# Optimization experiments

Hardware: AMD Instinct MI355X
Metric: run time of the kernel (lower is better)

## Reference

```python
import jax, jax.numpy as jnp
import numpy as np

N_NODES = 50000
N_EDGES = 800000
IN_DIM = 256
HID = 64
NEG_SLOPE = 0.2


def setup_inputs() -> dict:
    key = jax.random.key(0)
    ks = jax.random.split(key, 16)
    s = lambda d: 1.0 / np.sqrt(d)
    x = jax.random.normal(ks[0], (N_NODES, IN_DIM), dtype=jnp.float32)
    src = jax.random.randint(ks[1], (N_EDGES,), 0, N_NODES, dtype=jnp.int32)
    dst = jax.random.randint(ks[2], (N_EDGES,), 0, N_NODES, dtype=jnp.int32)
    # layer 0: in 256 -> 4 heads x 64, no residual, ELU
    W0 = jax.random.normal(ks[3], (IN_DIM, 4 * HID), dtype=jnp.float32) * s(IN_DIM)
    al0 = jax.random.normal(ks[4], (4, HID), dtype=jnp.float32) * s(HID)
    ar0 = jax.random.normal(ks[5], (4, HID), dtype=jnp.float32) * s(HID)
    b0 = jnp.zeros((4 * HID,), dtype=jnp.float32)
    # layer 1: in 256 -> 4 heads x 64, identity residual (256 == 4*64), ELU
    W1 = jax.random.normal(ks[6], (4 * HID, 4 * HID), dtype=jnp.float32) * s(4 * HID)
    al1 = jax.random.normal(ks[7], (4, HID), dtype=jnp.float32) * s(HID)
    ar1 = jax.random.normal(ks[8], (4, HID), dtype=jnp.float32) * s(HID)
    b1 = jnp.zeros((4 * HID,), dtype=jnp.float32)
    # layer 2 (output): in 256 -> 1 head x 64, linear residual, no activation
    W2 = jax.random.normal(ks[9], (4 * HID, HID), dtype=jnp.float32) * s(4 * HID)
    al2 = jax.random.normal(ks[10], (1, HID), dtype=jnp.float32) * s(HID)
    ar2 = jax.random.normal(ks[11], (1, HID), dtype=jnp.float32) * s(HID)
    b2 = jnp.zeros((HID,), dtype=jnp.float32)
    res_w2 = jax.random.normal(ks[12], (4 * HID, HID), dtype=jnp.float32) * s(4 * HID)
    return {"x": x, "src": src, "dst": dst,
            "W0": W0, "al0": al0, "ar0": ar0, "b0": b0,
            "W1": W1, "al1": al1, "ar1": ar1, "b1": b1,
            "W2": W2, "al2": al2, "ar2": ar2, "b2": b2,
            "res_w2": res_w2}


def gat_layer(h, src, dst, W, al, ar, bias, residual, res_w, activation):
    H, D = al.shape
    feat = (h @ W).reshape(-1, H, D)               # [N,H,D]
    el = jnp.sum(feat * al[None], axis=-1)         # [N,H]
    er = jnp.sum(feat * ar[None], axis=-1)         # [N,H]
    e = jax.nn.leaky_relu(el[src] + er[dst], NEG_SLOPE)  # [E,H]
    # segment softmax over incoming edges of each destination node
    emax = jax.ops.segment_max(e, dst, num_segments=N_NODES)  # [N,H]
    ee = jnp.exp(e - emax[dst])
    denom = jax.ops.segment_sum(ee, dst, num_segments=N_NODES)
    alpha = ee / denom[dst]                        # [E,H]
    msg = feat[src] * alpha[..., None]             # [E,H,D]
    out = jax.ops.segment_sum(msg, dst, num_segments=N_NODES)  # [N,H,D]
    if residual:
        if res_w is not None:
            out = out + (h @ res_w).reshape(-1, 1, D)
        else:
            out = out + h.reshape(-1, H, D)
    out = out + bias.reshape(H, D)
    if activation:
        out = jax.nn.elu(out)
    return out.reshape(-1, H * D)                  # flatten(1)


def reference(x, src, dst, W0, al0, ar0, b0, W1, al1, ar1, b1,
              W2, al2, ar2, b2, res_w2):
    h = gat_layer(x, src, dst, W0, al0, ar0, b0, False, None, True)
    h = gat_layer(h, src, dst, W1, al1, ar1, b1, True, None, True)
    h = gat_layer(h, src, dst, W2, al2, ar2, b2, True, res_w2, False)
    return h  # [N, 64]
```

## Files before the change

### kernel.cpp

```cpp
#include <hip/hip_runtime.h>
#include <math.h>

#define NNODES 50000
#define NEDGES 800000
#define NSB 49
#define NPACK 640
#define NCVT 3125
#define EBH 3125
#define NBM 391
#define SCB 1563

__device__ __forceinline__ float leaky(float x) { return x > 0.f ? x : 0.2f * x; }

__device__ __forceinline__ ushort f2bf(float f) {
    unsigned u = __float_as_uint(f);
    return (ushort)((u + 0x7fffu + ((u >> 16) & 1u)) >> 16);
}
__device__ __forceinline__ float bf2f(ushort u) {
    return __uint_as_float((unsigned)u << 16);
}

typedef const __attribute__((address_space(1))) void* gptr_t;
typedef __attribute__((address_space(3))) void* lptr_t;

__global__ __launch_bounds__(256) void front_kernel(
    const int* __restrict__ dst, int* __restrict__ counts,
    const float* __restrict__ W0, const float* __restrict__ W1, const float* __restrict__ W2,
    const float* __restrict__ Wr, ushort* __restrict__ Bt0, ushort* __restrict__ Bt1,
    ushort* __restrict__ Bt2, const float* __restrict__ x, ushort* __restrict__ xb) {
    using ushort8v = __attribute__((ext_vector_type(8))) unsigned short;
    int t = threadIdx.x;
    if (blockIdx.x < EBH) {
        int e = blockIdx.x * 256 + t;
        if (e < NEDGES) atomicAdd(&counts[dst[e]], 1);
    } else if (blockIdx.x < EBH + NPACK) {
        int idx = (blockIdx.x - EBH) * 256 + t;
        if (idx < 65536) {
            int n = idx >> 8, k = idx & 255;
            Bt0[idx] = f2bf(W0[k * 256 + n]);
        } else if (idx < 131072) {
            int j = idx - 65536;
            int n = j >> 8, k = j & 255;
            Bt1[j] = f2bf(W1[k * 256 + n]);
        } else {
            int j = idx - 131072;
            int n = j >> 8, k = j & 255;
            Bt2[j] = f2bf(n < 64 ? W2[k * 64 + n] : Wr[k * 64 + (n - 64)]);
        }
    } else {
        size_t j = (size_t)(blockIdx.x - EBH - NPACK) * 4096 + t * 16;
        float4 a0 = *reinterpret_cast<const float4*>(x + j);
        float4 a1 = *reinterpret_cast<const float4*>(x + j + 4);
        float4 a2 = *reinterpret_cast<const float4*>(x + j + 8);
        float4 a3 = *reinterpret_cast<const float4*>(x + j + 12);
        union { ushort8v v; ushort u[8]; } p0, p1;
        p0.u[0] = f2bf(a0.x); p0.u[1] = f2bf(a0.y); p0.u[2] = f2bf(a0.z); p0.u[3] = f2bf(a0.w);
        p0.u[4] = f2bf(a1.x); p0.u[5] = f2bf(a1.y); p0.u[6] = f2bf(a1.z); p0.u[7] = f2bf(a1.w);
        p1.u[0] = f2bf(a2.x); p1.u[1] = f2bf(a2.y); p1.u[2] = f2bf(a2.z); p1.u[3] = f2bf(a2.w);
        p1.u[4] = f2bf(a3.x); p1.u[5] = f2bf(a3.y); p1.u[6] = f2bf(a3.z); p1.u[7] = f2bf(a3.w);
        *reinterpret_cast<ushort8v*>(xb + j) = p0.v;
        *reinterpret_cast<ushort8v*>(xb + j + 8) = p1.v;
    }
}

__global__ __launch_bounds__(256) void scan_partial(const int* __restrict__ counts,
                                                    int* __restrict__ bsum, int Nn) {
    int b = blockIdx.x, t = threadIdx.x;
    int base = b * 1024;
    int v = 0;
#pragma unroll
    for (int i = 0; i < 4; ++i) {
        int idx = base + t + 256 * i;
        if (idx < Nn) v += counts[idx];
    }
    for (int o = 32; o; o >>= 1) v += __shfl_xor(v, o);
    __shared__ int ws[4];
    if ((t & 63) == 0) ws[t >> 6] = v;
    __syncthreads();
    if (t == 0) bsum[b] = ws[0] + ws[1] + ws[2] + ws[3];
}

__global__ __launch_bounds__(256) void scan_final(const int* __restrict__ counts,
                                                  const int* __restrict__ bsum,
                                                  int* __restrict__ row_start, int Nn, int nB) {
    __shared__ int off_s;
    __shared__ int tsum[256];
    int b = blockIdx.x, t = threadIdx.x;
    if (t == 0) {
        int o = 0;
        for (int i = 0; i < b; ++i) o += bsum[i];
        off_s = o;
    }
    int base = b * 1024 + t * 4;
    int c0 = 0, c1 = 0, c2 = 0, c3 = 0;
    if (base + 3 < Nn) {
        int4 c = *reinterpret_cast<const int4*>(counts + base);
        c0 = c.x; c1 = c.y; c2 = c.z; c3 = c.w;
    } else {
        if (base + 0 < Nn) c0 = counts[base + 0];
        if (base + 1 < Nn) c1 = counts[base + 1];
        if (base + 2 < Nn) c2 = counts[base + 2];
        if (base + 3 < Nn) c3 = counts[base + 3];
    }
    int s0 = c0, s1 = s0 + c1, s2 = s1 + c2, s3 = s2 + c3;
    tsum[t] = s3;
    __syncthreads();
    for (int o = 1; o < 256; o <<= 1) {
        int u = (t >= o) ? tsum[t - o] : 0;
        __syncthreads();
        tsum[t] += u;
        __syncthreads();
    }
    int o = off_s + tsum[t] - s3;
    if (base + 3 < Nn) {
        *reinterpret_cast<int4*>(row_start + base) = make_int4(o, o + s0, o + s1, o + s2);
    } else {
        if (base + 0 < Nn) row_start[base + 0] = o;
        if (base + 1 < Nn) row_start[base + 1] = o + s0;
        if (base + 2 < Nn) row_start[base + 2] = o + s1;
        if (base + 3 < Nn) row_start[base + 3] = o + s2;
    }
    if (b == nB - 1 && t == 255) row_start[Nn] = off_s + tsum[255];
}

template <bool SCAT>
__global__ __launch_bounds__(512) void gemm_wide(const ushort* __restrict__ Ab,
                                                 const ushort* __restrict__ Bt,
                                                 const float* __restrict__ al,
                                                 const float* __restrict__ ar,
                                                 ushort* __restrict__ featb,
                                                 float* __restrict__ el, float* __restrict__ er,
                                                 int Nrows,
                                                 const int* __restrict__ srcv,
                                                 const int* __restrict__ dstv,
                                                 const int* __restrict__ row_start,
                                                 int* __restrict__ cursor,
                                                 int* __restrict__ csr_src) {
    using bf16x8 = __attribute__((ext_vector_type(8))) short;
    using f32x4 = __attribute__((ext_vector_type(4))) float;
    __shared__ ushort As[8192];
    __shared__ ushort Bs[16384];
    if constexpr (SCAT) {
        if (blockIdx.x >= NBM) {
            int e = (blockIdx.x - NBM) * 512 + threadIdx.x;
            if (e < NEDGES) {
                int d = dstv[e];
                int pos = row_start[d] + atomicAdd(&cursor[d], 1);
                csr_src[pos] = srcv[e];
            }
            return;
        }
    }
    const int tid = threadIdx.x;
    const int lane = tid & 63;
    const int wave = tid >> 6;
    const int wr = wave >> 2, wc = wave & 3;
    const int q = lane >> 4, li = lane & 15;
    const int r0 = blockIdx.x * 128;

    f32x4 acc[4][4];
#pragma unroll
    for (int i = 0; i < 4; ++i)
#pragma unroll
        for (int j = 0; j < 4; ++j) acc[i][j] = (f32x4){0.f, 0.f, 0.f, 0.f};

    for (int kk = 0; kk < 256; kk += 64) {
        __syncthreads();
#pragma unroll
        for (int j = 0; j < 2; ++j) {
            int c = wave * 128 + j * 64 + lane;
            int mr = c & 15, kg = (c >> 4) & 7, mf = c >> 7;
            const ushort* gp = Ab + (size_t)(r0 + mf * 16 + mr) * 256 + kk + kg * 8;
            void* lp = (char*)As + (size_t)(wave * 2 + j) * 1024;
            __builtin_amdgcn_global_load_lds((gptr_t)gp, (lptr_t)lp, 16, 0, 0);
        }
#pragma unroll
        for (int j = 0; j < 4; ++j) {
            int c = wave * 256 + j * 64 + lane;
            int nr = c & 15, kg = (c >> 4) & 7, nf = c >> 7;
            const ushort* gp = Bt + (size_t)(nf * 16 + nr) * 256 + kk + kg * 8;
            void* lp = (char*)Bs + (size_t)(wave * 4 + j) * 1024;
            __builtin_amdgcn_global_load_lds((gptr_t)gp, (lptr_t)lp, 16, 0, 0);
        }
        __syncthreads();
#pragma unroll
        for (int t = 0; t < 2; ++t) {
            const int kc = t * 4 + q;
            bf16x8 af[4], bfv[4];
#pragma unroll
            for (int f = 0; f < 4; ++f) {
                af[f] = *reinterpret_cast<const bf16x8*>(
                    &As[(((wr * 4 + f) * 8 + kc) * 16 + li) * 8]);
                bfv[f] = *reinterpret_cast<const bf16x8*>(
                    &Bs[(((wc * 4 + f) * 8 + kc) * 16 + li) * 8]);
            }
#pragma unroll
            for (int f = 0; f < 4; ++f)
#pragma unroll
                for (int f2 = 0; f2 < 4; ++f2)
                    acc[f][f2] =
                        __builtin_amdgcn_mfma_f32_16x16x32_bf16(af[f], bfv[f2], acc[f][f2], 0, 0, 0);
        }
    }

    float alv[4], arv[4];
#pragma unroll
    for (int f2 = 0; f2 < 4; ++f2) {
        alv[f2] = al[wc * 64 + f2 * 16 + li];
        arv[f2] = ar[wc * 64 + f2 * 16 + li];
    }
#pragma unroll
    for (int f = 0; f < 4; ++f) {
#pragma unroll
        for (int r = 0; r < 4; ++r) {
            int row = r0 + wr * 64 + f * 16 + q * 4 + r;
            bool ok = row < Nrows;
            float elp = 0.f, erp = 0.f;
#pragma unroll
            for (int f2 = 0; f2 < 4; ++f2) {
                float v = acc[f][f2][r];
                elp = fmaf(v, alv[f2], elp);
                erp = fmaf(v, arv[f2], erp);
                if (ok) featb[(size_t)row * 256 + (f2 * 16 + li) * 4 + wc] = f2bf(v);
            }
#pragma unroll
            for (int o = 1; o < 16; o <<= 1) {
                elp += __shfl_xor(elp, o);
                erp += __shfl_xor(erp, o);
            }
            if (ok && li == 0) {
                el[row * 4 + wc] = elp;
                er[row * 4 + wc] = erp;
            }
        }
    }
}

__global__ __launch_bounds__(256) void gemm_l2(const ushort* __restrict__ Ab,
                                               const ushort* __restrict__ Bt,
                                               const float* __restrict__ al,
                                               const float* __restrict__ ar,
                                               ushort* __restrict__ featb,
                                               float* __restrict__ el, float* __restrict__ er,
                                               float* __restrict__ resid, int Nrows) {
    using bf16x8 = __attribute__((ext_vector_type(8))) short;
    using f32x4 = __attribute__((ext_vector_type(4))) float;
    __shared__ ushort As[8192];
    __shared__ ushort Bs[8192];
    const int tid = threadIdx.x;
    const int lane = tid & 63;
    const int wave = tid >> 6;
    const int wr = wave >> 1, wc = wave & 1;
    const int q = lane >> 4, li = lane & 15;
    const int r0 = blockIdx.x * 128;

    f32x4 acc[4][4];
#pragma unroll
    for (int i = 0; i < 4; ++i)
#pragma unroll
        for (int j = 0; j < 4; ++j) acc[i][j] = (f32x4){0.f, 0.f, 0.f, 0.f};

    for (int kk = 0; kk < 256; kk += 64) {
        __syncthreads();
#pragma unroll
        for (int j = 0; j < 4; ++j) {
            int c = (wave * 4 + j) * 64 + lane;
            int mr = c & 15, kg = (c >> 4) & 7, mf = c >> 7;
            const ushort* gp = Ab + (size_t)(r0 + mf * 16 + mr) * 256 + kk + kg * 8;
            void* lp = (char*)As + (size_t)(wave * 4 + j) * 1024;
            __builtin_amdgcn_global_load_lds((gptr_t)gp, (lptr_t)lp, 16, 0, 0);
        }
#pragma unroll
        for (int j = 0; j < 4; ++j) {
            int c = (wave * 4 + j) * 64 + lane;
            int nr = c & 15, kg = (c >> 4) & 7, nf = c >> 7;
            const ushort* gp = Bt + (size_t)(nf * 16 + nr) * 256 + kk + kg * 8;
            void* lp = (char*)Bs + (size_t)(wave * 4 + j) * 1024;
            __builtin_amdgcn_global_load_lds((gptr_t)gp, (lptr_t)lp, 16, 0, 0);
        }
        __syncthreads();
#pragma unroll
        for (int t = 0; t < 2; ++t) {
            const int kc = t * 4 + q;
            bf16x8 af[4], bfv[4];
#pragma unroll
            for (int f = 0; f < 4; ++f) {
                af[f] = *reinterpret_cast<const bf16x8*>(
                    &As[(((wr * 4 + f) * 8 + kc) * 16 + li) * 8]);
                bfv[f] = *reinterpret_cast<const bf16x8*>(
                    &Bs[(((wc * 4 + f) * 8 + kc) * 16 + li) * 8]);
            }
#pragma unroll
            for (int f = 0; f < 4; ++f)
#pragma unroll
                for (int f2 = 0; f2 < 4; ++f2)
                    acc[f][f2] =
                        __builtin_amdgcn_mfma_f32_16x16x32_bf16(af[f], bfv[f2], acc[f][f2], 0, 0, 0);
        }
    }

    if (wc == 0) {
        float alv[4], arv[4];
#pragma unroll
        for (int f2 = 0; f2 < 4; ++f2) {
            alv[f2] = al[f2 * 16 + li];
            arv[f2] = ar[f2 * 16 + li];
        }
#pragma unroll
        for (int f = 0; f < 4; ++f) {
#pragma unroll
            for (int r = 0; r < 4; ++r) {
                int row = r0 + wr * 64 + f * 16 + q * 4 + r;
                bool ok = row < Nrows;
                float elp = 0.f, erp = 0.f;
#pragma unroll
                for (int f2 = 0; f2 < 4; ++f2) {
                    float v = acc[f][f2][r];
                    elp = fmaf(v, alv[f2], elp);
                    erp = fmaf(v, arv[f2], erp);
                    if (ok) featb[(size_t)row * 64 + f2 * 16 + li] = f2bf(v);
                }
#pragma unroll
                for (int o = 1; o < 16; o <<= 1) {
                    elp += __shfl_xor(elp, o);
                    erp += __shfl_xor(erp, o);
                }
                if (ok && li == 0) {
                    el[row] = elp;
                    er[row] = erp;
                }
            }
        }
    } else {
#pragma unroll
        for (int f = 0; f < 4; ++f) {
#pragma unroll
            for (int r = 0; r < 4; ++r) {
                int row = r0 + wr * 64 + f * 16 + q * 4 + r;
                if (row < Nrows) {
#pragma unroll
                    for (int f2 = 0; f2 < 4; ++f2)
                        resid[(size_t)row * 64 + f2 * 16 + li] = acc[f][f2][r];
                }
            }
        }
    }
}

template <int RES, bool ACT>
__global__ __launch_bounds__(256) void agg4_kernel(
    const ushort* __restrict__ featb, const float* __restrict__ el,
    const float* __restrict__ er, const int* __restrict__ row_start,
    const int* __restrict__ csr_src, const ushort* __restrict__ resbuf,
    const float* __restrict__ bias, ushort* __restrict__ out, int Nn) {
    using ushort8v = __attribute__((ext_vector_type(8))) unsigned short;
    __shared__ float wbuf[4][256];
    __shared__ int obuf[4][64];
    const int wv = threadIdx.x >> 6, lane = threadIdx.x & 63;
    const int g = lane >> 5, li = lane & 31;
    int node = blockIdx.x * 4 + wv;
    if (node >= Nn) return;

    int begin = row_start[node], end = row_start[node + 1];
    float4 ern = *(reinterpret_cast<const float4*>(er) + node);

    float denom[4] = {0.f, 0.f, 0.f, 0.f};
    float acc[2][4] = {{0.f, 0.f, 0.f, 0.f}, {0.f, 0.f, 0.f, 0.f}};

    for (int c = begin; c < end; c += 64) {
        int nE = min(64, end - c);
        float4 w = make_float4(0.f, 0.f, 0.f, 0.f);
        int s = 0;
        if (lane < nE) {
            s = csr_src[c + lane];
            float4 e4 = *(reinterpret_cast<const float4*>(el) + s);
            w.x = __expf(leaky(e4.x + ern.x));
            w.y = __expf(leaky(e4.y + ern.y));
            w.z = __expf(leaky(e4.z + ern.z));
            w.w = __expf(leaky(e4.w + ern.w));
        }
        denom[0] += w.x; denom[1] += w.y; denom[2] += w.z; denom[3] += w.w;
        obuf[wv][lane] = s * 256;
        *reinterpret_cast<float4*>(&wbuf[wv][lane * 4]) = w;
        __asm__ volatile("s_waitcnt lgkmcnt(0)" ::: "memory");

#pragma unroll 4
        for (int e2 = 0; e2 < nE; e2 += 2) {
            int e = e2 + g;
            float4 we = make_float4(0.f, 0.f, 0.f, 0.f);
            int off = 0;
            if (e < nE) {
                off = obuf[wv][e];
                we = *reinterpret_cast<const float4*>(&wbuf[wv][e * 4]);
            }
            ushort8v v = *reinterpret_cast<const ushort8v*>(featb + off + li * 8);
            acc[0][0] = fmaf(we.x, bf2f(v[0]), acc[0][0]);
            acc[0][1] = fmaf(we.y, bf2f(v[1]), acc[0][1]);
            acc[0][2] = fmaf(we.z, bf2f(v[2]), acc[0][2]);
            acc[0][3] = fmaf(we.w, bf2f(v[3]), acc[0][3]);
            acc[1][0] = fmaf(we.x, bf2f(v[4]), acc[1][0]);
            acc[1][1] = fmaf(we.y, bf2f(v[5]), acc[1][1]);
            acc[1][2] = fmaf(we.z, bf2f(v[6]), acc[1][2]);
            acc[1][3] = fmaf(we.w, bf2f(v[7]), acc[1][3]);
        }
        __asm__ volatile("" ::: "memory");
    }

#pragma unroll
    for (int j = 0; j < 2; ++j)
#pragma unroll
        for (int h = 0; h < 4; ++h) acc[j][h] += __shfl_xor(acc[j][h], 32);
#pragma unroll
    for (int h = 0; h < 4; ++h)
        for (int o = 32; o; o >>= 1) denom[h] += __shfl_xor(denom[h], o);

    bool has = end > begin;
#pragma unroll
    for (int hh = 0; hh < 2; ++hh) {
        int h = g * 2 + hh;
        float d0 = denom[h];
        float o0 = has ? acc[0][h] / d0 : 0.f;
        float o1 = has ? acc[1][h] / d0 : 0.f;
        int dbase = h * 64 + li * 2;
        if constexpr (RES == 1) {
            unsigned rv = *reinterpret_cast<const unsigned*>(resbuf + (size_t)node * 256 + dbase);
            o0 += bf2f((ushort)(rv & 0xffffu));
            o1 += bf2f((ushort)(rv >> 16));
        }
        float2 bv = *reinterpret_cast<const float2*>(bias + dbase);
        o0 += bv.x; o1 += bv.y;
        if constexpr (ACT) {
            o0 = o0 > 0.f ? o0 : __expf(o0) - 1.f;
            o1 = o1 > 0.f ? o1 : __expf(o1) - 1.f;
        }
        unsigned pk = (unsigned)f2bf(o0) | ((unsigned)f2bf(o1) << 16);
        *reinterpret_cast<unsigned*>(out + (size_t)node * 256 + dbase) = pk;
    }
}

__global__ __launch_bounds__(256) void agg1_kernel(
    const ushort* __restrict__ featb, const float* __restrict__ el,
    const float* __restrict__ er, const int* __restrict__ row_start,
    const int* __restrict__ csr_src, const float* __restrict__ resbuf,
    const float* __restrict__ bias, float* __restrict__ out, int Nn) {
    __shared__ float wbuf[4][64];
    __shared__ int obuf[4][64];
    const int wv = threadIdx.x >> 6, lane = threadIdx.x & 63;
    const int g = lane >> 4, li = lane & 15;
    int node = blockIdx.x * 4 + wv;
    if (node >= Nn) return;

    int begin = row_start[node], end = row_start[node + 1];
    float ern = er[node];
    float denom = 0.f;
    float acc[4] = {0.f, 0.f, 0.f, 0.f};

    for (int c = begin; c < end; c += 64) {
        int nE = min(64, end - c);
        float w = 0.f;
        int s = 0;
        if (lane < nE) {
            s = csr_src[c + lane];
            w = __expf(leaky(el[s] + ern));
        }
        denom += w;
        obuf[wv][lane] = s * 64;
        wbuf[wv][lane] = w;
        __asm__ volatile("s_waitcnt lgkmcnt(0)" ::: "memory");

#pragma unroll 2
        for (int e4i = 0; e4i < nE; e4i += 4) {
            int e = e4i + g;
            float we = 0.f;
            int off = 0;
            if (e < nE) {
                off = obuf[wv][e];
                we = wbuf[wv][e];
            }
            ushort4 v = *reinterpret_cast<const ushort4*>(featb + off + li * 4);
            acc[0] = fmaf(we, bf2f(v.x), acc[0]);
            acc[1] = fmaf(we, bf2f(v.y), acc[1]);
            acc[2] = fmaf(we, bf2f(v.z), acc[2]);
            acc[3] = fmaf(we, bf2f(v.w), acc[3]);
        }
        __asm__ volatile("" ::: "memory");
    }

#pragma unroll
    for (int j = 0; j < 4; ++j) {
        acc[j] += __shfl_xor(acc[j], 16);
        acc[j] += __shfl_xor(acc[j], 32);
    }
    for (int o = 32; o; o >>= 1) denom += __shfl_xor(denom, o);

    if (g == 0) {
        bool has = end > begin;
        float4 rv = *reinterpret_cast<const float4*>(resbuf + (size_t)node * 64 + li * 4);
        float4 bv = *reinterpret_cast<const float4*>(bias + li * 4);
        float4 o4;
        o4.x = (has ? acc[0] / denom : 0.f) + rv.x + bv.x;
        o4.y = (has ? acc[1] / denom : 0.f) + rv.y + bv.y;
        o4.z = (has ? acc[2] / denom : 0.f) + rv.z + bv.z;
        o4.w = (has ? acc[3] / denom : 0.f) + rv.w + bv.w;
        *reinterpret_cast<float4*>(out + (size_t)node * 64 + li * 4) = o4;
    }
}

extern "C" void kernel_launch(void* const* d_in, const int* in_sizes, int n_in, void* d_out,
                              int out_size, void* d_ws, size_t ws_size, hipStream_t stream) {
    const float* x   = (const float*)d_in[0];
    const int* src   = (const int*)d_in[1];
    const int* dst   = (const int*)d_in[2];
    const float* W0  = (const float*)d_in[3];
    const float* al0 = (const float*)d_in[4];
    const float* ar0 = (const float*)d_in[5];
    const float* b0  = (const float*)d_in[6];
    const float* W1  = (const float*)d_in[7];
    const float* al1 = (const float*)d_in[8];
    const float* ar1 = (const float*)d_in[9];
    const float* b1  = (const float*)d_in[10];
    const float* W2  = (const float*)d_in[11];
    const float* al2 = (const float*)d_in[12];
    const float* ar2 = (const float*)d_in[13];
    const float* b2  = (const float*)d_in[14];
    const float* Wr2 = (const float*)d_in[15];
    float* out = (float*)d_out;

    char* w = (char*)d_ws;
    size_t off = 0;
    auto alloc = [&](size_t bytes) -> char* {
        char* p = w + off;
        off += (bytes + 255) & ~(size_t)255;
        return p;
    };
    ushort* xb      = (ushort*)alloc((size_t)NNODES * 256 * 2);
    ushort* hbuf    = (ushort*)alloc((size_t)NNODES * 256 * 2);
    ushort* featb   = (ushort*)alloc((size_t)NNODES * 256 * 2);
    float* resid    = (float*)alloc((size_t)NNODES * 64 * 4);
    float* el       = (float*)alloc((size_t)NNODES * 4 * 4);
    float* er       = (float*)alloc((size_t)NNODES * 4 * 4);
    ushort* Bt0     = (ushort*)alloc(65536 * 2);
    ushort* Bt1     = (ushort*)alloc(65536 * 2);
    ushort* Bt2     = (ushort*)alloc(32768 * 2);
    int* counts     = (int*)alloc((size_t)NNODES * 4 * 2);
    int* cursor     = counts + NNODES;
    int* row_start  = (int*)alloc((size_t)(NNODES + 1) * 4);
    int* bsum       = (int*)alloc(64 * 4);
    int* csr_src    = (int*)alloc((size_t)NEDGES * 4);

    hipMemsetAsync(counts, 0, (size_t)NNODES * 4 * 2, stream);

    const int NB4 = (NNODES + 3) / 4;

    front_kernel<<<EBH + NPACK + NCVT, 256, 0, stream>>>(dst, counts, W0, W1, W2, Wr2,
                                                         Bt0, Bt1, Bt2, x, xb);
    scan_partial<<<NSB, 256, 0, stream>>>(counts, bsum, NNODES);
    scan_final<<<NSB, 256, 0, stream>>>(counts, bsum, row_start, NNODES, NSB);

    gemm_wide<true><<<NBM + SCB, 512, 0, stream>>>(xb, Bt0, al0, ar0, featb, el, er, NNODES,
                                                   src, dst, row_start, cursor, csr_src);
    agg4_kernel<0, true><<<NB4, 256, 0, stream>>>(featb, el, er, row_start, csr_src,
                                                  nullptr, b0, hbuf, NNODES);
    gemm_wide<false><<<NBM, 512, 0, stream>>>(hbuf, Bt1, al1, ar1, featb, el, er, NNODES,
                                              nullptr, nullptr, nullptr, nullptr, nullptr);
    agg4_kernel<1, true><<<NB4, 256, 0, stream>>>(featb, el, er, row_start, csr_src,
                                                  hbuf, b1, hbuf, NNODES);
    gemm_l2<<<NBM, 256, 0, stream>>>(hbuf, Bt2, al2, ar2, featb, el, er, resid, NNODES);
    agg1_kernel<<<NB4, 256, 0, stream>>>(featb, el, er, row_start, csr_src,
                                         resid, b2, out, NNODES);
}
```

Baseline: 419.4 us.

## Store features in column slabs and split aggregation by column group per XCD

Node features and the bf16 input are stored as 8 column slabs of 32 channels each, instead of row-major 256-wide rows. The GEMM loads and stores are re-indexed to match. The aggregation kernels now launch one block per (16-node group, column slab), with the slab chosen by blockIdx&7. Each block therefore gathers from a 3.2MB slab, which should fit in cache and, with round-robin block dispatch, mostly map to one XCD's L2. CSR source indices shrink to 16-bit to cut index traffic. In exchange, the edge-softmax weights (exp) are recomputed once per slab, and the 16-bit indices only work because there are fewer than 65536 nodes.

Result: slower. 629.1 us (+50.0%).

```diff
diff --git a/kernel.cpp b/kernel.cpp
--- a/kernel.cpp
+++ b/kernel.cpp
@@ -9,6 +9,8 @@
 #define EBH 3125
 #define NBM 391
 #define SCB 1563
+#define AGG4B 25000
+#define AGG1B 6250
 
 __device__ __forceinline__ float leaky(float x) { return x > 0.f ? x : 0.2f * x; }
 
@@ -22,6 +24,7 @@
 
 typedef const __attribute__((address_space(1))) void* gptr_t;
 typedef __attribute__((address_space(3))) void* lptr_t;
+
 
 __global__ __launch_bounds__(256) void front_kernel(
     const int* __restrict__ dst, int* __restrict__ counts,
@@ -49,6 +52,8 @@
         }
     } else {
         size_t j = (size_t)(blockIdx.x - EBH - NPACK) * 4096 + t * 16;
+        int node = (int)(j >> 8);
+        int c0 = (int)(j & 255);
         float4 a0 = *reinterpret_cast<const float4*>(x + j);
         float4 a1 = *reinterpret_cast<const float4*>(x + j + 4);
         float4 a2 = *reinterpret_cast<const float4*>(x + j + 8);
@@ -58,8 +63,11 @@
         p0.u[4] = f2bf(a1.x); p0.u[5] = f2bf(a1.y); p0.u[6] = f2bf(a1.z); p0.u[7] = f2bf(a1.w);
         p1.u[0] = f2bf(a2.x); p1.u[1] = f2bf(a2.y); p1.u[2] = f2bf(a2.z); p1.u[3] = f2bf(a2.w);
         p1.u[4] = f2bf(a3.x); p1.u[5] = f2bf(a3.y); p1.u[6] = f2bf(a3.z); p1.u[7] = f2bf(a3.w);
-        *reinterpret_cast<ushort8v*>(xb + j) = p0.v;
-        *reinterpret_cast<ushort8v*>(xb + j + 8) = p1.v;
+        int c1 = c0 + 8;
+        size_t o0 = ((size_t)((c0 >> 3) & 7) * NNODES + node) * 32 + ((c0 >> 6) << 3);
+        size_t o1 = ((size_t)((c1 >> 3) & 7) * NNODES + node) * 32 + ((c1 >> 6) << 3);
+        *reinterpret_cast<ushort8v*>(xb + o0) = p0.v;
+        *reinterpret_cast<ushort8v*>(xb + o1) = p1.v;
     }
 }
 
@@ -135,7 +143,7 @@
                                                  const int* __restrict__ dstv,
                                                  const int* __restrict__ row_start,
                                                  int* __restrict__ cursor,
-                                                 int* __restrict__ csr_src) {
+                                                 ushort* __restrict__ csr_src) {
     using bf16x8 = __attribute__((ext_vector_type(8))) short;
     using f32x4 = __attribute__((ext_vector_type(4))) float;
     __shared__ ushort As[8192];
@@ -146,7 +154,7 @@
             if (e < NEDGES) {
                 int d = dstv[e];
                 int pos = row_start[d] + atomicAdd(&cursor[d], 1);
-                csr_src[pos] = srcv[e];
+                csr_src[pos] = (ushort)srcv[e];
             }
             return;
         }
@@ -170,7 +178,9 @@
         for (int j = 0; j < 2; ++j) {
             int c = wave * 128 + j * 64 + lane;
             int mr = c & 15, kg = (c >> 4) & 7, mf = c >> 7;
-            const ushort* gp = Ab + (size_t)(r0 + mf * 16 + mr) * 256 + kk + kg * 8;
+            int k0 = kk + kg * 8;
+            int row = r0 + mf * 16 + mr;
+            const ushort* gp = Ab + ((size_t)((k0 >> 3) & 7) * NNODES + row) * 32 + ((k0 >> 6) << 3);
             void* lp = (char*)As + (size_t)(wave * 2 + j) * 1024;
             __builtin_amdgcn_global_load_lds((gptr_t)gp, (lptr_t)lp, 16, 0, 0);
         }
@@ -221,7 +231,8 @@
                 float v = acc[f][f2][r];
                 elp = fmaf(v, alv[f2], elp);
                 erp = fmaf(v, arv[f2], erp);
-                if (ok) featb[(size_t)row * 256 + (f2 * 16 + li) * 4 + wc] = f2bf(v);
+                int cc = (f2 * 16 + li) * 4 + wc;
+                if (ok) featb[((size_t)(cc >> 5) * NNODES + row) * 32 + (cc & 31)] = f2bf(v);
             }
 #pragma unroll
             for (int o = 1; o < 16; o <<= 1) {
@@ -266,7 +277,9 @@
         for (int j = 0; j < 4; ++j) {
             int c = (wave * 4 + j) * 64 + lane;
             int mr = c & 15, kg = (c >> 4) & 7, mf = c >> 7;
-            const ushort* gp = Ab + (size_t)(r0 + mf * 16 + mr) * 256 + kk + kg * 8;
+            int k0 = kk + kg * 8;
+            int row = r0 + mf * 16 + mr;
+            const ushort* gp = Ab + ((size_t)((k0 >> 3) & 7) * NNODES + row) * 32 + ((k0 >> 6) << 3);
             void* lp = (char*)As + (size_t)(wave * 4 + j) * 1024;
             __builtin_amdgcn_global_load_lds((gptr_t)gp, (lptr_t)lp, 16, 0, 0);
         }
@@ -318,7 +331,8 @@
                     float v = acc[f][f2][r];
                     elp = fmaf(v, alv[f2], elp);
                     erp = fmaf(v, arv[f2], erp);
-                    if (ok) featb[(size_t)row * 64 + f2 * 16 + li] = f2bf(v);
+                    int cc = f2 * 16 + li;
+                    if (ok) featb[((size_t)(cc >> 5) * NNODES + row) * 32 + (cc & 31)] = f2bf(v);
                 }
 #pragma unroll
                 for (int o = 1; o < 16; o <<= 1) {
@@ -348,161 +362,150 @@
 }
 
 template <int RES, bool ACT>
-__global__ __launch_bounds__(256) void agg4_kernel(
+__global__ __launch_bounds__(256) void agg4s_kernel(
     const ushort* __restrict__ featb, const float* __restrict__ el,
     const float* __restrict__ er, const int* __restrict__ row_start,
-    const int* __restrict__ csr_src, const ushort* __restrict__ resbuf,
-    const float* __restrict__ bias, ushort* __restrict__ out, int Nn) {
-    using ushort8v = __attribute__((ext_vector_type(8))) unsigned short;
-    __shared__ float wbuf[4][256];
+    const ushort* __restrict__ csr_src, const ushort* __restrict__ resbuf,
+    const float* __restrict__ bias, ushort* __restrict__ out) {
+    __shared__ float4 wbuf[4][64];
     __shared__ int obuf[4][64];
     const int wv = threadIdx.x >> 6, lane = threadIdx.x & 63;
-    const int g = lane >> 5, li = lane & 31;
-    int node = blockIdx.x * 4 + wv;
-    if (node >= Nn) return;
-
-    int begin = row_start[node], end = row_start[node + 1];
-    float4 ern = *(reinterpret_cast<const float4*>(er) + node);
-
-    float denom[4] = {0.f, 0.f, 0.f, 0.f};
-    float acc[2][4] = {{0.f, 0.f, 0.f, 0.f}, {0.f, 0.f, 0.f, 0.f}};
-
-    for (int c = begin; c < end; c += 64) {
-        int nE = min(64, end - c);
-        float4 w = make_float4(0.f, 0.f, 0.f, 0.f);
-        int s = 0;
-        if (lane < nE) {
-            s = csr_src[c + lane];
-            float4 e4 = *(reinterpret_cast<const float4*>(el) + s);
-            w.x = __expf(leaky(e4.x + ern.x));
-            w.y = __expf(leaky(e4.y + ern.y));
-            w.z = __expf(leaky(e4.z + ern.z));
-            w.w = __expf(leaky(e4.w + ern.w));
-        }
-        denom[0] += w.x; denom[1] += w.y; denom[2] += w.z; denom[3] += w.w;
-        obuf[wv][lane] = s * 256;
-        *reinterpret_cast<float4*>(&wbuf[wv][lane * 4]) = w;
-        __asm__ volatile("s_waitcnt lgkmcnt(0)" ::: "memory");
-
+    const int g = lane >> 3, li = lane & 7;
+    const int cg = blockIdx.x & 7;
+    const int blk = blockIdx.x >> 3;
+    const ushort* fslab = featb + (size_t)cg * NNODES * 32 + li * 4;
+    float bv = 0.f;
+    if (lane < 32) bv = bias[(lane >> 3) * 64 + cg * 8 + (lane & 7)];
+
+    for (int rep = 0; rep < 4; ++rep) {
+        const int node = blk * 16 + wv * 4 + rep;
+        const int begin = row_start[node], end = row_start[node + 1];
+        const float4 ern = *(reinterpret_cast<const float4*>(er) + node);
+        float dn[4] = {0.f, 0.f, 0.f, 0.f};
+        float acc[4] = {0.f, 0.f, 0.f, 0.f};
+        for (int c = begin; c < end; c += 64) {
+            int nE = min(64, end - c);
+            float4 w = make_float4(0.f, 0.f, 0.f, 0.f);
+            int s = 0;
+            if (lane < nE) {
+                s = csr_src[c + lane];
+                float4 e4 = *(reinterpret_cast<const float4*>(el) + s);
+                w.x = __expf(leaky(e4.x + ern.x));
+                w.y = __expf(leaky(e4.y + ern.y));
+                w.z = __expf(leaky(e4.z + ern.z));
+                w.w = __expf(leaky(e4.w + ern.w));
+            }
+            obuf[wv][lane] = s * 32;
+            wbuf[wv][lane] = w;
+            __asm__ volatile("s_waitcnt lgkmcnt(0)" ::: "memory");
 #pragma unroll 4
-        for (int e2 = 0; e2 < nE; e2 += 2) {
-            int e = e2 + g;
-            float4 we = make_float4(0.f, 0.f, 0.f, 0.f);
-            int off = 0;
-            if (e < nE) {
-                off = obuf[wv][e];
-                we = *reinterpret_cast<const float4*>(&wbuf[wv][e * 4]);
-            }
-            ushort8v v = *reinterpret_cast<const ushort8v*>(featb + off + li * 8);
-            acc[0][0] = fmaf(we.x, bf2f(v[0]), acc[0][0]);
-            acc[0][1] = fmaf(we.y, bf2f(v[1]), acc[0][1]);
-            acc[0][2] = fmaf(we.z, bf2f(v[2]), acc[0][2]);
-            acc[0][3] = fmaf(we.w, bf2f(v[3]), acc[0][3]);
-            acc[1][0] = fmaf(we.x, bf2f(v[4]), acc[1][0]);
-            acc[1][1] = fmaf(we.y, bf2f(v[5]), acc[1][1]);
-            acc[1][2] = fmaf(we.z, bf2f(v[6]), acc[1][2]);
-            acc[1][3] = fmaf(we.w, bf2f(v[7]), acc[1][3]);
-        }
-        __asm__ volatile("" ::: "memory");
-    }
-
-#pragma unroll
-    for (int j = 0; j < 2; ++j)
-#pragma unroll
-        for (int h = 0; h < 4; ++h) acc[j][h] += __shfl_xor(acc[j][h], 32);
-#pragma unroll
-    for (int h = 0; h < 4; ++h)
-        for (int o = 32; o; o >>= 1) denom[h] += __shfl_xor(denom[h], o);
-
-    bool has = end > begin;
-#pragma unroll
-    for (int hh = 0; hh < 2; ++hh) {
-        int h = g * 2 + hh;
-        float d0 = denom[h];
-        float o0 = has ? acc[0][h] / d0 : 0.f;
-        float o1 = has ? acc[1][h] / d0 : 0.f;
-        int dbase = h * 64 + li * 2;
-        if constexpr (RES == 1) {
-            unsigned rv = *reinterpret_cast<const unsigned*>(resbuf + (size_t)node * 256 + dbase);
-            o0 += bf2f((ushort)(rv & 0xffffu));
-            o1 += bf2f((ushort)(rv >> 16));
-        }
-        float2 bv = *reinterpret_cast<const float2*>(bias + dbase);
-        o0 += bv.x; o1 += bv.y;
-        if constexpr (ACT) {
-            o0 = o0 > 0.f ? o0 : __expf(o0) - 1.f;
-            o1 = o1 > 0.f ? o1 : __expf(o1) - 1.f;
-        }
-        unsigned pk = (unsigned)f2bf(o0) | ((unsigned)f2bf(o1) << 16);
-        *reinterpret_cast<unsigned*>(out + (size_t)node * 256 + dbase) = pk;
-    }
-}
-
-__global__ __launch_bounds__(256) void agg1_kernel(
+            for (int e8 = 0; e8 < nE; e8 += 8) {
+                int e = e8 + g;
+                float4 we = make_float4(0.f, 0.f, 0.f, 0.f);
+                int off = 0;
+                if (e < nE) {
+                    off = obuf[wv][e];
+                    we = wbuf[wv][e];
+                }
+                ushort4 v = *reinterpret_cast<const ushort4*>(fslab + off);
+                dn[0] += we.x; dn[1] += we.y; dn[2] += we.z; dn[3] += we.w;
+                acc[0] = fmaf(we.x, bf2f(v.x), acc[0]);
+                acc[1] = fmaf(we.y, bf2f(v.y), acc[1]);
+                acc[2] = fmaf(we.z, bf2f(v.z), acc[2]);
+                acc[3] = fmaf(we.w, bf2f(v.w), acc[3]);
+            }
+            __asm__ volatile("" ::: "memory");
+        }
+#pragma unroll
+        for (int h = 0; h < 4; ++h) {
+            acc[h] += __shfl_xor(acc[h], 8);
+            acc[h] += __shfl_xor(acc[h], 16);
+            acc[h] += __shfl_xor(acc[h], 32);
+            dn[h] += __shfl_xor(dn[h], 8);
+            dn[h] += __shfl_xor(dn[h], 16);
+            dn[h] += __shfl_xor(dn[h], 32);
+        }
+        if (lane < 32) {
+            const int h = lane >> 3;
+            float o = (end > begin) ? acc[h] * __builtin_amdgcn_rcpf(dn[h]) : 0.f;
+            size_t oidx = ((size_t)cg * NNODES + node) * 32 + lane;
+            if constexpr (RES == 1) o += bf2f(resbuf[oidx]);
+            o += bv;
+            if constexpr (ACT) o = o > 0.f ? o : __expf(o) - 1.f;
+            out[oidx] = f2bf(o);
+        }
+    }
+}
+
+__global__ __launch_bounds__(256) void agg1s_kernel(
     const ushort* __restrict__ featb, const float* __restrict__ el,
     const float* __restrict__ er, const int* __restrict__ row_start,
-    const int* __restrict__ csr_src, const float* __restrict__ resbuf,
-    const float* __restrict__ bias, float* __restrict__ out, int Nn) {
+    const ushort* __restrict__ csr_src, const float* __restrict__ resbuf,
+    const float* __restrict__ bias, float* __restrict__ out) {
     __shared__ float wbuf[4][64];
     __shared__ int obuf[4][64];
     const int wv = threadIdx.x >> 6, lane = threadIdx.x & 63;
-    const int g = lane >> 4, li = lane & 15;
-    int node = blockIdx.x * 4 + wv;
-    if (node >= Nn) return;
-
-    int begin = row_start[node], end = row_start[node + 1];
-    float ern = er[node];
-    float denom = 0.f;
-    float acc[4] = {0.f, 0.f, 0.f, 0.f};
-
-    for (int c = begin; c < end; c += 64) {
-        int nE = min(64, end - c);
-        float w = 0.f;
-        int s = 0;
-        if (lane < nE) {
-            s = csr_src[c + lane];
-            w = __expf(leaky(el[s] + ern));
-        }
-        denom += w;
-        obuf[wv][lane] = s * 64;
-        wbuf[wv][lane] = w;
-        __asm__ volatile("s_waitcnt lgkmcnt(0)" ::: "memory");
-
-#pragma unroll 2
-        for (int e4i = 0; e4i < nE; e4i += 4) {
-            int e = e4i + g;
-            float we = 0.f;
-            int off = 0;
-            if (e < nE) {
-                off = obuf[wv][e];
-                we = wbuf[wv][e];
-            }
-            ushort4 v = *reinterpret_cast<const ushort4*>(featb + off + li * 4);
-            acc[0] = fmaf(we, bf2f(v.x), acc[0]);
-            acc[1] = fmaf(we, bf2f(v.y), acc[1]);
-            acc[2] = fmaf(we, bf2f(v.z), acc[2]);
-            acc[3] = fmaf(we, bf2f(v.w), acc[3]);
-        }
-        __asm__ volatile("" ::: "memory");
-    }
-
-#pragma unroll
-    for (int j = 0; j < 4; ++j) {
-        acc[j] += __shfl_xor(acc[j], 16);
-        acc[j] += __shfl_xor(acc[j], 32);
-    }
-    for (int o = 32; o; o >>= 1) denom += __shfl_xor(denom, o);
-
-    if (g == 0) {
-        bool has = end > begin;
-        float4 rv = *reinterpret_cast<const float4*>(resbuf + (size_t)node * 64 + li * 4);
-        float4 bv = *reinterpret_cast<const float4*>(bias + li * 4);
-        float4 o4;
-        o4.x = (has ? acc[0] / denom : 0.f) + rv.x + bv.x;
-        o4.y = (has ? acc[1] / denom : 0.f) + rv.y + bv.y;
-        o4.z = (has ? acc[2] / denom : 0.f) + rv.z + bv.z;
-        o4.w = (has ? acc[3] / denom : 0.f) + rv.w + bv.w;
-        *reinterpret_cast<float4*>(out + (size_t)node * 64 + li * 4) = o4;
+    const int g = lane >> 3, li = lane & 7;
+    const int cg = blockIdx.x & 1;
+    const int blk = blockIdx.x >> 1;
+    const ushort* fslab = featb + (size_t)cg * NNODES * 32 + li * 4;
+    float4 bv = make_float4(0.f, 0.f, 0.f, 0.f);
+    if (lane < 8) bv = *reinterpret_cast<const float4*>(bias + cg * 32 + lane * 4);
+
+    for (int rep = 0; rep < 4; ++rep) {
+        const int node = blk * 16 + wv * 4 + rep;
+        const int begin = row_start[node], end = row_start[node + 1];
+        const float ern = er[node];
+        float dn = 0.f;
+        float acc[4] = {0.f, 0.f, 0.f, 0.f};
+        for (int c = begin; c < end; c += 64) {
+            int nE = min(64, end - c);
+            float w = 0.f;
+            int s = 0;
+            if (lane < nE) {
+                s = csr_src[c + lane];
+                w = __expf(leaky(el[s] + ern));
+            }
+            obuf[wv][lane] = s * 32;
+            wbuf[wv][lane] = w;
+            __asm__ volatile("s_waitcnt lgkmcnt(0)" ::: "memory");
+#pragma unroll 4
+            for (int e8 = 0; e8 < nE; e8 += 8) {
+                int e = e8 + g;
+                float we = 0.f;
+                int off = 0;
+                if (e < nE) {
+                    off = obuf[wv][e];
+                    we = wbuf[wv][e];
+                }
+                ushort4 v = *reinterpret_cast<const ushort4*>(fslab + off);
+                dn += we;
+                acc[0] = fmaf(we, bf2f(v.x), acc[0]);
+                acc[1] = fmaf(we, bf2f(v.y), acc[1]);
+                acc[2] = fmaf(we, bf2f(v.z), acc[2]);
+                acc[3] = fmaf(we, bf2f(v.w), acc[3]);
+            }
+            __asm__ volatile("" ::: "memory");
+        }
+#pragma unroll
+        for (int j = 0; j < 4; ++j) {
+            acc[j] += __shfl_xor(acc[j], 8);
+            acc[j] += __shfl_xor(acc[j], 16);
+            acc[j] += __shfl_xor(acc[j], 32);
+        }
+        dn += __shfl_xor(dn, 8);
+        dn += __shfl_xor(dn, 16);
+        dn += __shfl_xor(dn, 32);
+        if (lane < 8) {
+            float inv = (end > begin) ? __builtin_amdgcn_rcpf(dn) : 0.f;
+            float4 rv = *reinterpret_cast<const float4*>(resbuf + (size_t)node * 64 + cg * 32 + lane * 4);
+            float4 o4;
+            o4.x = acc[0] * inv + rv.x + bv.x;
+            o4.y = acc[1] * inv + rv.y + bv.y;
+            o4.z = acc[2] * inv + rv.z + bv.z;
+            o4.w = acc[3] * inv + rv.w + bv.w;
+            *reinterpret_cast<float4*>(out + (size_t)node * 64 + cg * 32 + lane * 4) = o4;
+        }
     }
 }
 
@@ -546,11 +549,9 @@
     int* cursor     = counts + NNODES;
     int* row_start  = (int*)alloc((size_t)(NNODES + 1) * 4);
     int* bsum       = (int*)alloc(64 * 4);
-    int* csr_src    = (int*)alloc((size_t)NEDGES * 4);
+    ushort* csr_src = (ushort*)alloc((size_t)NEDGES * 2);
 
     hipMemsetAsync(counts, 0, (size_t)NNODES * 4 * 2, stream);
-
-    const int NB4 = (NNODES + 3) / 4;
 
     front_kernel<<<EBH + NPACK + NCVT, 256, 0, stream>>>(dst, counts, W0, W1, W2, Wr2,
                                                          Bt0, Bt1, Bt2, x, xb);
@@ -559,13 +560,13 @@
 
     gemm_wide<true><<<NBM + SCB, 512, 0, stream>>>(xb, Bt0, al0, ar0, featb, el, er, NNODES,
                                                    src, dst, row_start, cursor, csr_src);
-    agg4_kernel<0, true><<<NB4, 256, 0, stream>>>(featb, el, er, row_start, csr_src,
-                                                  nullptr, b0, hbuf, NNODES);
+    agg4s_kernel<0, true><<<AGG4B, 256, 0, stream>>>(featb, el, er, row_start, csr_src,
+                                                     nullptr, b0, hbuf);
     gemm_wide<false><<<NBM, 512, 0, stream>>>(hbuf, Bt1, al1, ar1, featb, el, er, NNODES,
                                               nullptr, nullptr, nullptr, nullptr, nullptr);
-    agg4_kernel<1, true><<<NB4, 256, 0, stream>>>(featb, el, er, row_start, csr_src,
-                                                  hbuf, b1, hbuf, NNODES);
+    agg4s_kernel<1, true><<<AGG4B, 256, 0, stream>>>(featb, el, er, row_start, csr_src,
+                                                     hbuf, b1, hbuf);
     gemm_l2<<<NBM, 256, 0, stream>>>(hbuf, Bt2, al2, ar2, featb, el, er, resid, NNODES);
-    agg1_kernel<<<NB4, 256, 0, stream>>>(featb, el, er, row_start, csr_src,
-                                         resid, b2, out, NNODES);
-}
+    agg1s_kernel<<<AGG1B, 256, 0, stream>>>(featb, el, er, row_start, csr_src,
+                                            resid, b2, out);
+}
```
